# Performance work log

Hardware: AMD Instinct MI355X
Metric: run time of the kernel (lower is better)

The kernel has to match this reference:

```python
import jax, jax.numpy as jnp
import numpy as np

D_MODEL = 1024

def setup_inputs() -> dict:
    key = jax.random.key(0)
    ks = jax.random.split(key, 7)
    B, T, D = 4, 4096, D_MODEL
    s = 1.0 / np.sqrt(D)
    return {
        "x": jax.random.normal(ks[0], (B, T, D), dtype=jnp.float32),
        "Wq": jax.random.normal(ks[1], (D, D), dtype=jnp.float32) * s,
        "bq": jax.random.normal(ks[2], (D,), dtype=jnp.float32) * 0.01,
        "Wk": jax.random.normal(ks[3], (D, D), dtype=jnp.float32) * s,
        "bk": jax.random.normal(ks[4], (D,), dtype=jnp.float32) * 0.01,
        "Wv": jax.random.normal(ks[5], (D, D), dtype=jnp.float32) * s,
        "bv": jax.random.normal(ks[6], (D,), dtype=jnp.float32) * 0.01,
    }

def reference(x, Wq, bq, Wk, bk, Wv, bv):
    # x: [B, T, D]; Linear weights stored [out, in] like torch -> x @ W.T + b
    D = x.shape[-1]
    T = x.shape[1]
    scale = jnp.sqrt(jnp.asarray(D, dtype=x.dtype))
    Q = jnp.einsum('btd,ed->bte', x, Wq) + bq
    K = jnp.einsum('btd,ed->bte', x, Wk) + bk
    V = jnp.einsum('btd,ed->bte', x, Wv) + bv
    scores = jnp.einsum('bqd,bkd->bqk', Q, K) / scale  # [B, T, T]
    causal = jnp.tril(jnp.ones((T, T), dtype=bool))    # True = keep (q >= k)
    neg_inf = jnp.asarray(-jnp.inf, dtype=scores.dtype)
    scores = jnp.where(causal, scores, neg_inf)
    probs = jax.nn.softmax(scores, axis=-1)
    return jnp.einsum('bqk,bkd->bqd', probs, V)
```

## Files before the change

### kernel.cpp

```cpp
#include <hip/hip_runtime.h>
#include <hip/hip_bf16.h>
#include <math.h>


typedef __bf16 bf16;
typedef __bf16 bf16x8 __attribute__((ext_vector_type(8)));
typedef float  f32x4  __attribute__((ext_vector_type(4)));

#define LOG2E 1.4426950408889634f

static constexpr size_t OFF_XB   = 0;
static constexpr size_t OFF_WQB  = 33554432;
static constexpr size_t OFF_WKB  = 35651584;
static constexpr size_t OFF_WVB  = 37748736;
static constexpr size_t OFF_Q    = 39845888;
static constexpr size_t OFF_K    = 73400320;
static constexpr size_t OFF_VT   = 106954752;
static constexpr size_t OFF_S    = 140509184;

typedef __attribute__((address_space(1))) void gvoid_t;
typedef __attribute__((address_space(3))) void lvoid_t;

__device__ __forceinline__ void gload16(const void* g, void* l) {
  __builtin_amdgcn_global_load_lds((gvoid_t*)g, (lvoid_t*)l, 16, 0, 0);
}

struct Ctx { int tid, lane, quad, col16, wr, wc; };
__device__ __forceinline__ Ctx mk_ctx() {
  Ctx c; c.tid = (int)threadIdx.x; c.lane = c.tid & 63;
  int w = c.tid >> 6;
  c.quad = c.lane >> 4; c.col16 = c.lane & 15;
  c.wr = (w >> 1) * 64; c.wc = (w & 1) * 64;
  return c;
}

__device__ __forceinline__ void stage_tile(const bf16* g, long ld, bf16* s, int tid) {
  int lane = tid & 63, w = tid >> 6;
  const bf16* gp = g + (long)(lane >> 2) * ld + (long)(lane & 3) * 8;
  long step = 16 * ld;
  gload16(gp + (long)(2 * w) * step,     s + (2 * w) * 512);
  gload16(gp + (long)(2 * w + 1) * step, s + (2 * w + 1) * 512);
}

__device__ __forceinline__ void mfma_step(const bf16* sA, const bf16* sB,
                                          const Ctx& c, f32x4 acc[4][4]) {
  bf16x8 a[4], b[4];
#pragma unroll
  for (int i = 0; i < 4; ++i) {
    a[i] = *(const bf16x8*)(sA + ((c.wr + i * 16 + c.col16) * 32 + c.quad * 8));
    b[i] = *(const bf16x8*)(sB + ((c.wc + i * 16 + c.col16) * 32 + c.quad * 8));
  }
#pragma unroll
  for (int i = 0; i < 4; ++i)
#pragma unroll
    for (int j = 0; j < 4; ++j)
      acc[i][j] = __builtin_amdgcn_mfma_f32_16x16x32_bf16(a[i], b[j], acc[i][j], 0, 0, 0);
}

__device__ __forceinline__ void zero_acc(f32x4 acc[4][4]) {
  f32x4 z = {0.f, 0.f, 0.f, 0.f};
#pragma unroll
  for (int i = 0; i < 4; ++i)
#pragma unroll
    for (int j = 0; j < 4; ++j) acc[i][j] = z;
}

__device__ __forceinline__ int tridec(int i) {
  int qt = (int)((sqrtf(8.0f * (float)i + 1.0f) - 1.0f) * 0.5f);
  while ((qt + 1) * (qt + 2) / 2 <= i) ++qt;
  while (qt * (qt + 1) / 2 > i) --qt;
  return qt;
}


__global__ __launch_bounds__(256) void cvtk(const float* __restrict__ in,
                                            bf16* __restrict__ out, long n) {
  long i = ((long)blockIdx.x * 256 + threadIdx.x) * 8;
  if (i + 8 > n) return;
  float4 f0 = *(const float4*)(in + i);
  float4 f1 = *(const float4*)(in + i + 4);
  bf16x8 h;
  h[0] = (bf16)f0.x; h[1] = (bf16)f0.y; h[2] = (bf16)f0.z; h[3] = (bf16)f0.w;
  h[4] = (bf16)f1.x; h[5] = (bf16)f1.y; h[6] = (bf16)f1.z; h[7] = (bf16)f1.w;
  *(bf16x8*)(out + i) = h;
}

__global__ __launch_bounds__(256) void qk_gemm(const bf16* __restrict__ X,
                                               const bf16* __restrict__ Wq,
                                               const bf16* __restrict__ Wk,
                                               const float* __restrict__ bq,
                                               const float* __restrict__ bk,
                                               bf16* __restrict__ Q,
                                               bf16* __restrict__ K) {
  __shared__ __align__(16) bf16 sA[128 * 32], sB[128 * 32];
  Ctx c = mk_ctx();
  const bf16*  W    = blockIdx.z ? Wk : Wq;
  const float* bias = blockIdx.z ? bk : bq;
  bf16*        out  = blockIdx.z ? K : Q;
  long r0 = (long)blockIdx.y * 128, c0 = (long)blockIdx.x * 128;
  f32x4 acc[4][4]; zero_acc(acc);
  for (int k = 0; k < 1024; k += 32) {
    stage_tile(X + r0 * 1024 + k, 1024, sA, c.tid);
    stage_tile(W + c0 * 1024 + k, 1024, sB, c.tid);
    __syncthreads();
    mfma_step(sA, sB, c, acc);
    __syncthreads();
  }
#pragma unroll
  for (int j = 0; j < 4; ++j) {
    int col = c.wc + j * 16 + c.col16;
    float bb = bias[c0 + col];
#pragma unroll
    for (int i = 0; i < 4; ++i) {
      int rowb = c.wr + i * 16 + c.quad * 4;
#pragma unroll
      for (int r = 0; r < 4; ++r)
        out[(r0 + rowb + r) * 1024 + c0 + col] = (bf16)(acc[i][j][r] + bb);
    }
  }
}

__global__ __launch_bounds__(256) void vt_gemm(const bf16* __restrict__ X,
                                               const bf16* __restrict__ Wv,
                                               const float* __restrict__ bv,
                                               bf16* __restrict__ Vt) {
  __shared__ __align__(16) bf16 sA[128 * 32], sB[128 * 32];
  Ctx c = mk_ctx();
  int z = blockIdx.z;
  long r0 = (long)blockIdx.y * 128;
  long c0 = (long)blockIdx.x * 128;
  const bf16* Ab = Wv + r0 * 1024;
  const bf16* Bb = X + (long)z * 4194304 + c0 * 1024;
  f32x4 acc[4][4]; zero_acc(acc);
  for (int k = 0; k < 1024; k += 32) {
    stage_tile(Ab + k, 1024, sA, c.tid);
    stage_tile(Bb + k, 1024, sB, c.tid);
    __syncthreads();
    mfma_step(sA, sB, c, acc);
    __syncthreads();
  }
  bf16* out = Vt + (long)z * 4194304;
#pragma unroll
  for (int i = 0; i < 4; ++i) {
    int rowb = c.wr + i * 16 + c.quad * 4;
    float bb[4];
#pragma unroll
    for (int r = 0; r < 4; ++r) bb[r] = bv[r0 + rowb + r];
#pragma unroll
    for (int j = 0; j < 4; ++j) {
      int col = c.wc + j * 16 + c.col16;
#pragma unroll
      for (int r = 0; r < 4; ++r)
        out[(r0 + rowb + r) * 4096 + c0 + col] = (bf16)(acc[i][j][r] + bb[r]);
    }
  }
}

__global__ __launch_bounds__(256) void s_gemm(const bf16* __restrict__ Q,
                                              const bf16* __restrict__ K,
                                              bf16* __restrict__ S) {
  __shared__ __align__(16) bf16 sA[128 * 32], sB[128 * 32];
  Ctx c = mk_ctx();
  int ti = blockIdx.x, z = blockIdx.z;
  int qt = tridec(ti);
  int kt = ti - qt * (qt + 1) / 2;
  long q0 = (long)qt * 128, k0 = (long)kt * 128;
  const bf16* Ab = Q + (long)z * 4194304 + q0 * 1024;
  const bf16* Bb = K + (long)z * 4194304 + k0 * 1024;
  f32x4 acc[4][4]; zero_acc(acc);
  for (int k = 0; k < 1024; k += 32) {
    stage_tile(Ab + k, 1024, sA, c.tid);
    stage_tile(Bb + k, 1024, sB, c.tid);
    __syncthreads();
    mfma_step(sA, sB, c, acc);
    __syncthreads();
  }
  bf16* st = S + ((long)z * 528 + ti) * 16384;
  const bool diag = (qt == kt);
#pragma unroll
  for (int i = 0; i < 4; ++i) {
#pragma unroll
    for (int r = 0; r < 4; ++r) {
      int row_l = c.wr + i * 16 + c.quad * 4 + r;
#pragma unroll
      for (int j = 0; j < 4; ++j) {
        int col_l = c.wc + j * 16 + c.col16;
        float p = exp2f(acc[i][j][r] * (0.03125f * LOG2E));
        if (diag && col_l > row_l) p = 0.0f;
        st[row_l * 128 + col_l] = (bf16)p;
      }
    }
  }
}

__global__ __launch_bounds__(256) void norm_rows(bf16* __restrict__ S) {
  int row = blockIdx.x & 4095, z = blockIdx.x >> 12;
  int qt = row >> 7, r = row & 127;
  int n = (qt + 1) << 7;
  bf16* base = S + ((long)z * 528 + (long)qt * (qt + 1) / 2) * 16384 + (long)r * 128;
  int tid = (int)threadIdx.x;
  bf16x8 v[2];
  float s = 0.f;
  int cnt = 0;
  for (int e = tid * 8; e < n; e += 2048) {
    bf16x8 x = *(const bf16x8*)(base + (long)(e >> 7) * 16384 + (e & 127));
    v[cnt++] = x;
#pragma unroll
    for (int jj = 0; jj < 8; ++jj) s += (float)x[jj];
  }
#pragma unroll
  for (int m = 1; m <= 32; m <<= 1) s += __shfl_xor(s, m);
  __shared__ float red[4];
  if ((tid & 63) == 0) red[tid >> 6] = s;
  __syncthreads();
  float li = 1.0f / (red[0] + red[1] + red[2] + red[3]);
  cnt = 0;
  for (int e = tid * 8; e < n; e += 2048) {
    bf16x8 x = v[cnt++];
#pragma unroll
    for (int jj = 0; jj < 8; ++jj) x[jj] = (bf16)((float)x[jj] * li);
    *(bf16x8*)(base + (long)(e >> 7) * 16384 + (e & 127)) = x;
  }
}

__global__ __launch_bounds__(256) void o_gemm(const bf16* __restrict__ S,
                                              const bf16* __restrict__ Vt,
                                              float* __restrict__ out) {
  __shared__ __align__(16) bf16 sA[128 * 32], sB[128 * 32];
  Ctx c = mk_ctx();
  int et = blockIdx.x, qt = blockIdx.y, z = blockIdx.z;
  long q0 = (long)qt * 128, e0 = (long)et * 128;
  const bf16* Bb = Vt + (long)z * 4194304 + e0 * 4096;
  long tribase = ((long)z * 528 + (long)qt * (qt + 1) / 2) * 16384;
  f32x4 acc[4][4]; zero_acc(acc);
  int kend = (qt + 1) * 128;
  for (int k = 0; k < kend; k += 32) {
    const bf16* Ab = S + tribase + (long)(k >> 7) * 16384 + (k & 127);
    stage_tile(Ab, 128, sA, c.tid);
    stage_tile(Bb + k, 4096, sB, c.tid);
    __syncthreads();
    mfma_step(sA, sB, c, acc);
    __syncthreads();
  }
#pragma unroll
  for (int i = 0; i < 4; ++i) {
    int rowb = c.wr + i * 16 + c.quad * 4;
#pragma unroll
    for (int j = 0; j < 4; ++j) {
      int col = c.wc + j * 16 + c.col16;
#pragma unroll
      for (int r = 0; r < 4; ++r)
        out[((long)z * 4096 + q0 + rowb + r) * 1024 + e0 + col] = acc[i][j][r];
    }
  }
}

extern "C" void kernel_launch(void* const* d_in, const int* in_sizes, int n_in,
                              void* d_out, int out_size, void* d_ws, size_t ws_size,
                              hipStream_t stream) {
  (void)in_sizes; (void)n_in; (void)out_size; (void)ws_size;
  const float* x  = (const float*)d_in[0];
  const float* Wq = (const float*)d_in[1];
  const float* bq = (const float*)d_in[2];
  const float* Wk = (const float*)d_in[3];
  const float* bk = (const float*)d_in[4];
  const float* Wv = (const float*)d_in[5];
  const float* bv = (const float*)d_in[6];

  char* ws = (char*)d_ws;
  bf16* xb  = (bf16*)(ws + OFF_XB);
  bf16* wqb = (bf16*)(ws + OFF_WQB);
  bf16* wkb = (bf16*)(ws + OFF_WKB);
  bf16* wvb = (bf16*)(ws + OFF_WVB);
  bf16* Qb  = (bf16*)(ws + OFF_Q);
  bf16* Kb  = (bf16*)(ws + OFF_K);
  bf16* Vtb = (bf16*)(ws + OFF_VT);
  bf16* Sb  = (bf16*)(ws + OFF_S);

  cvtk<<<8192, 256, 0, stream>>>(x,  xb,  16777216L);
  cvtk<<<512,  256, 0, stream>>>(Wq, wqb, 1048576L);
  cvtk<<<512,  256, 0, stream>>>(Wk, wkb, 1048576L);
  cvtk<<<512,  256, 0, stream>>>(Wv, wvb, 1048576L);

  qk_gemm<<<dim3(8, 128, 2), 256, 0, stream>>>(xb, wqb, wkb, bq, bk, Qb, Kb);
  vt_gemm<<<dim3(32, 8, 4), 256, 0, stream>>>(xb, wvb, bv, Vtb);
  s_gemm<<<dim3(528, 1, 4), 256, 0, stream>>>(Qb, Kb, Sb);
  norm_rows<<<16384, 256, 0, stream>>>(Sb);
  o_gemm<<<dim3(8, 32, 4), 256, 0, stream>>>(Sb, Vtb, (float*)d_out);
}
```

Baseline: 599.0 us.

## Fuse row-sum into score GEMM and defer softmax normalization to output

Computes per-tile partial row sums of the exponentiated scores inside s_gemm and writes them to a small buffer. A tiny kernel reduces them to inverse sums, which o_gemm applies in its epilogue. This removes the separate norm_rows pass that read and rewrote the whole bf16 score matrix. It also reverses the o_gemm query-tile order so the longest causal tiles launch first, which should improve load balance.

```diff
diff --git a/kernel.cpp b/kernel.cpp
--- a/kernel.cpp
+++ b/kernel.cpp
@@ -17,6 +17,8 @@
 static constexpr size_t OFF_K    = 73400320;
 static constexpr size_t OFF_VT   = 106954752;
 static constexpr size_t OFF_S    = 140509184;
+static constexpr size_t OFF_PSUM = 209715200;
+static constexpr size_t OFF_LINV = 211812352;
 
 typedef __attribute__((address_space(1))) void gvoid_t;
 typedef __attribute__((address_space(3))) void lvoid_t;
@@ -25,12 +27,12 @@
   __builtin_amdgcn_global_load_lds((gvoid_t*)g, (lvoid_t*)l, 16, 0, 0);
 }
 
-struct Ctx { int tid, lane, quad, col16, wr, wc; };
+struct Ctx { int tid, lane, quad, col16, wr, wc, wcol; };
 __device__ __forceinline__ Ctx mk_ctx() {
   Ctx c; c.tid = (int)threadIdx.x; c.lane = c.tid & 63;
   int w = c.tid >> 6;
   c.quad = c.lane >> 4; c.col16 = c.lane & 15;
-  c.wr = (w >> 1) * 64; c.wc = (w & 1) * 64;
+  c.wr = (w >> 1) * 64; c.wc = (w & 1) * 64; c.wcol = w & 1;
   return c;
 }
 
@@ -158,8 +160,10 @@
 
 __global__ __launch_bounds__(256) void s_gemm(const bf16* __restrict__ Q,
                                               const bf16* __restrict__ K,
-                                              bf16* __restrict__ S) {
+                                              bf16* __restrict__ S,
+                                              float* __restrict__ psum) {
   __shared__ __align__(16) bf16 sA[128 * 32], sB[128 * 32];
+  __shared__ float sred[2][128];
   Ctx c = mk_ctx();
   int ti = blockIdx.x, z = blockIdx.z;
   int qt = tridec(ti);
@@ -177,58 +181,62 @@
   }
   bf16* st = S + ((long)z * 528 + ti) * 16384;
   const bool diag = (qt == kt);
+  float rs[4][4];
 #pragma unroll
   for (int i = 0; i < 4; ++i) {
 #pragma unroll
     for (int r = 0; r < 4; ++r) {
       int row_l = c.wr + i * 16 + c.quad * 4 + r;
+      float s = 0.f;
 #pragma unroll
       for (int j = 0; j < 4; ++j) {
         int col_l = c.wc + j * 16 + c.col16;
         float p = exp2f(acc[i][j][r] * (0.03125f * LOG2E));
         if (diag && col_l > row_l) p = 0.0f;
-        st[row_l * 128 + col_l] = (bf16)p;
+        bf16 h = (bf16)p;
+        st[row_l * 128 + col_l] = h;
+        s += (float)h;
       }
+      rs[i][r] = s;
     }
   }
-}
-
-__global__ __launch_bounds__(256) void norm_rows(bf16* __restrict__ S) {
-  int row = blockIdx.x & 4095, z = blockIdx.x >> 12;
-  int qt = row >> 7, r = row & 127;
-  int n = (qt + 1) << 7;
-  bf16* base = S + ((long)z * 528 + (long)qt * (qt + 1) / 2) * 16384 + (long)r * 128;
-  int tid = (int)threadIdx.x;
-  bf16x8 v[2];
-  float s = 0.f;
-  int cnt = 0;
-  for (int e = tid * 8; e < n; e += 2048) {
-    bf16x8 x = *(const bf16x8*)(base + (long)(e >> 7) * 16384 + (e & 127));
-    v[cnt++] = x;
-#pragma unroll
-    for (int jj = 0; jj < 8; ++jj) s += (float)x[jj];
-  }
-#pragma unroll
-  for (int m = 1; m <= 32; m <<= 1) s += __shfl_xor(s, m);
-  __shared__ float red[4];
-  if ((tid & 63) == 0) red[tid >> 6] = s;
+#pragma unroll
+  for (int i = 0; i < 4; ++i)
+#pragma unroll
+    for (int r = 0; r < 4; ++r)
+#pragma unroll
+      for (int m = 1; m <= 8; m <<= 1)
+        rs[i][r] += __shfl_xor(rs[i][r], m);
+  if (c.col16 == 0) {
+#pragma unroll
+    for (int i = 0; i < 4; ++i)
+#pragma unroll
+      for (int r = 0; r < 4; ++r)
+        sred[c.wcol][c.wr + i * 16 + c.quad * 4 + r] = rs[i][r];
+  }
   __syncthreads();
-  float li = 1.0f / (red[0] + red[1] + red[2] + red[3]);
-  cnt = 0;
-  for (int e = tid * 8; e < n; e += 2048) {
-    bf16x8 x = v[cnt++];
-#pragma unroll
-    for (int jj = 0; jj < 8; ++jj) x[jj] = (bf16)((float)x[jj] * li);
-    *(bf16x8*)(base + (long)(e >> 7) * 16384 + (e & 127)) = x;
-  }
+  if (c.tid < 128)
+    psum[((long)z * 4096 + q0 + c.tid) * 32 + kt] = sred[0][c.tid] + sred[1][c.tid];
+}
+
+__global__ __launch_bounds__(256) void inv_sums(const float* __restrict__ psum,
+                                                float* __restrict__ linv) {
+  long i = (long)blockIdx.x * 256 + threadIdx.x;
+  int q = (int)(i & 4095);
+  int nt = (q >> 7) + 1;
+  const float* ps = psum + i * 32;
+  float l = 0.f;
+  for (int t = 0; t < nt; ++t) l += ps[t];
+  linv[i] = 1.0f / l;
 }
 
 __global__ __launch_bounds__(256) void o_gemm(const bf16* __restrict__ S,
                                               const bf16* __restrict__ Vt,
+                                              const float* __restrict__ linv,
                                               float* __restrict__ out) {
   __shared__ __align__(16) bf16 sA[128 * 32], sB[128 * 32];
   Ctx c = mk_ctx();
-  int et = blockIdx.x, qt = blockIdx.y, z = blockIdx.z;
+  int et = blockIdx.x, qt = 31 - (int)blockIdx.y, z = blockIdx.z;
   long q0 = (long)qt * 128, e0 = (long)et * 128;
   const bf16* Bb = Vt + (long)z * 4194304 + e0 * 4096;
   long tribase = ((long)z * 528 + (long)qt * (qt + 1) / 2) * 16384;
@@ -242,15 +250,19 @@
     mfma_step(sA, sB, c, acc);
     __syncthreads();
   }
+  long zq = (long)z * 4096 + q0;
 #pragma unroll
   for (int i = 0; i < 4; ++i) {
     int rowb = c.wr + i * 16 + c.quad * 4;
+    float li[4];
+#pragma unroll
+    for (int r = 0; r < 4; ++r) li[r] = linv[zq + rowb + r];
 #pragma unroll
     for (int j = 0; j < 4; ++j) {
       int col = c.wc + j * 16 + c.col16;
 #pragma unroll
       for (int r = 0; r < 4; ++r)
-        out[((long)z * 4096 + q0 + rowb + r) * 1024 + e0 + col] = acc[i][j][r];
+        out[(zq + rowb + r) * 1024 + e0 + col] = acc[i][j][r] * li[r];
     }
   }
 }
@@ -268,14 +280,16 @@
   const float* bv = (const float*)d_in[6];
 
   char* ws = (char*)d_ws;
-  bf16* xb  = (bf16*)(ws + OFF_XB);
-  bf16* wqb = (bf16*)(ws + OFF_WQB);
-  bf16* wkb = (bf16*)(ws + OFF_WKB);
-  bf16* wvb = (bf16*)(ws + OFF_WVB);
-  bf16* Qb  = (bf16*)(ws + OFF_Q);
-  bf16* Kb  = (bf16*)(ws + OFF_K);
-  bf16* Vtb = (bf16*)(ws + OFF_VT);
-  bf16* Sb  = (bf16*)(ws + OFF_S);
+  bf16*  xb   = (bf16*)(ws + OFF_XB);
+  bf16*  wqb  = (bf16*)(ws + OFF_WQB);
+  bf16*  wkb  = (bf16*)(ws + OFF_WKB);
+  bf16*  wvb  = (bf16*)(ws + OFF_WVB);
+  bf16*  Qb   = (bf16*)(ws + OFF_Q);
+  bf16*  Kb   = (bf16*)(ws + OFF_K);
+  bf16*  Vtb  = (bf16*)(ws + OFF_VT);
+  bf16*  Sb   = (bf16*)(ws + OFF_S);
+  float* psum = (float*)(ws + OFF_PSUM);
+  float* linv = (float*)(ws + OFF_LINV);
 
   cvtk<<<8192, 256, 0, stream>>>(x,  xb,  16777216L);
   cvtk<<<512,  256, 0, stream>>>(Wq, wqb, 1048576L);
@@ -284,7 +298,7 @@
 
   qk_gemm<<<dim3(8, 128, 2), 256, 0, stream>>>(xb, wqb, wkb, bq, bk, Qb, Kb);
   vt_gemm<<<dim3(32, 8, 4), 256, 0, stream>>>(xb, wvb, bv, Vtb);
-  s_gemm<<<dim3(528, 1, 4), 256, 0, stream>>>(Qb, Kb, Sb);
-  norm_rows<<<16384, 256, 0, stream>>>(Sb);
-  o_gemm<<<dim3(8, 32, 4), 256, 0, stream>>>(Sb, Vtb, (float*)d_out);
-}
+  s_gemm<<<dim3(528, 1, 4), 256, 0, stream>>>(Qb, Kb, Sb, psum);
+  inv_sums<<<64, 256, 0, stream>>>(psum, linv);
+  o_gemm<<<dim3(8, 32, 4), 256, 0, stream>>>(Sb, Vtb, linv, (float*)d_out);
+}
```

Result: faster. 547.6 us (-8.6%).
